# Kernel optimization log

Hardware: AMD Instinct MI355X
Metric: run time of the kernel (lower is better)

Reference implementation:

```python
import jax, jax.numpy as jnp
import numpy as np

SCORE_THRESHOLD = 0.5
NMS_TOP_K = 1024
NMS_THRESHOLD = 0.6
N_ANCHORS = 262144
N_CLASSES = 80


def setup_inputs() -> dict:
    key = jax.random.key(0)
    k1, k2, k3 = jax.random.split(key, 3)
    # valid xyxy boxes: x1<x2, y1<y2
    xy = jax.random.uniform(k1, (1, N_ANCHORS, 2), minval=0.0, maxval=2048.0)
    wh = jax.random.uniform(k2, (1, N_ANCHORS, 2), minval=1.0, maxval=64.0)
    pred_bboxes = jnp.concatenate([xy, xy + wh], axis=-1)  # [1, N, 4]
    pred_scores = jax.random.uniform(k3, (1, N_ANCHORS, N_CLASSES))  # [1, N, C]
    return {"pred_bboxes": pred_bboxes, "pred_scores": pred_scores}


def _pairwise_iou(boxes):
    # boxes: [K, 4] xyxy -> [K, K] IoU
    area = (boxes[:, 2] - boxes[:, 0]) * (boxes[:, 3] - boxes[:, 1])
    lt = jnp.maximum(boxes[:, None, :2], boxes[None, :, :2])
    rb = jnp.minimum(boxes[:, None, 2:], boxes[None, :, 2:])
    wh = jnp.clip(rb - lt, 0.0)
    inter = wh[..., 0] * wh[..., 1]
    union = area[:, None] + area[None, :] - inter
    return inter / jnp.maximum(union, 1e-9)


def reference(pred_bboxes, pred_scores):
    scores = pred_scores[0]  # [N, C]
    boxes = pred_bboxes[0]   # [N, 4]

    # single-label-per-box branch: per-anchor best class
    conf = jnp.max(scores, axis=1)      # [N]
    label = jnp.argmax(scores, axis=1)  # [N] int

    # score threshold (masking instead of data-dependent filtering)
    masked_conf = jnp.where(conf >= SCORE_THRESHOLD, conf, -1.0)

    # top-k candidates (sorted descending, matching torch.topk)
    top_conf, top_idx = jax.lax.top_k(masked_conf, NMS_TOP_K)  # [K]
    top_boxes = boxes[top_idx]   # [K, 4]
    top_label = label[top_idx]   # [K]
    valid = top_conf >= SCORE_THRESHOLD  # [K] rows that passed the threshold

    # batched_nms trick: offset boxes per class so cross-class IoU is ~0
    max_coord = jax.lax.stop_gradient(jnp.max(top_boxes)) + 1.0
    offset_boxes = top_boxes + top_label.astype(top_boxes.dtype)[:, None] * max_coord
    iou = _pairwise_iou(offset_boxes)  # [K, K]

    # sequential greedy suppression in score order (rows already sorted)
    idx = jnp.arange(NMS_TOP_K)

    def body(i, keep):
        suppress = (iou[i] > NMS_THRESHOLD) & (idx > i) & keep[i] & keep
        return keep & ~suppress

    keep = jax.lax.fori_loop(0, NMS_TOP_K, body, valid)  # [K] bool

    out = jnp.concatenate(
        [top_boxes, top_conf[:, None], top_label.astype(top_boxes.dtype)[:, None]],
        axis=1,
    )  # [K, 6] = [x1, y1, x2, y2, conf, label]
    # fixed-shape masked output: suppressed / invalid rows zeroed
    return out * keep[:, None].astype(out.dtype)
```

## Files before the change

### kernel.cpp

```cpp
#include <hip/hip_runtime.h>
#include <stdint.h>


#define N_ANCH   262144
#define N_CLS    80
#define K_TOP    1024
#define CAP      4096

typedef unsigned long long ull;

#define HSLOT(b) ((((b) & 2047u) << 4) | ((b) >> 11))
#define SKEW(e) ((uint32_t)(e) + ((uint32_t)(e) >> 4))

#define OFF_HIST  0
#define OFF_CTRL  131072
#define MEMSET_BYTES 131136
#define OFF_BINS  131136
#define OFF_LIST  655424
#define WS_REQUIRED 688192

__global__ __launch_bounds__(256) void k_sentinel(float* __restrict__ out, float v) {
    int i = blockIdx.x * 256 + threadIdx.x;
    if (i < K_TOP * 6) out[i] = v;
}

static __device__ __forceinline__ uint32_t conf_key24(float best) {
    uint32_t u = __float_as_uint(best);
    if (u > 0x3F800000u) u = 0x3F800000u;
    if (u < 0x3F000000u) u = 0x3F000000u;
    return u - 0x3F000000u;
}

static __device__ __forceinline__ void cmpsw(ull& x, ull& y, bool up) {
    ull mn = x < y ? x : y, mx = x < y ? y : x;
    x = up ? mn : mx; y = up ? mx : mn;
}

__global__ __launch_bounds__(256) void k_conf(const float* __restrict__ scores,
                                              uint16_t* __restrict__ bins16,
                                              uint32_t* __restrict__ hist) {
    const int t = threadIdx.x;
    const int r = t >> 4, s = t & 15;
    const int a0 = blockIdx.x * 128 + r;
    const float* base = scores + (size_t)a0 * N_CLS;
    float4 v0[4], v1[4];
    #pragma unroll
    for (int p = 0; p < 4; p++) {
        const float* nb = base + (size_t)p * 16 * N_CLS;
        v0[p] = ((const float4*)nb)[s];
        if (s < 4) v1[p] = ((const float4*)nb)[16 + s];
    }
    #pragma unroll
    for (int i = 0; i < 8; i++) {
        float4 c0 = v0[i & 3], c1 = v1[i & 3];
        if (i + 4 < 8) {
            const float* nb = base + (size_t)(i + 4) * 16 * N_CLS;
            v0[i & 3] = ((const float4*)nb)[s];
            if (s < 4) v1[i & 3] = ((const float4*)nb)[16 + s];
        }
        float best = c0.x; int lab = 4 * s;
        if (c0.y > best) { best = c0.y; lab = 4 * s + 1; }
        if (c0.z > best) { best = c0.z; lab = 4 * s + 2; }
        if (c0.w > best) { best = c0.w; lab = 4 * s + 3; }
        if (s < 4) {
            const int c = 64 + 4 * s;
            if (c1.x > best) { best = c1.x; lab = c; }
            if (c1.y > best) { best = c1.y; lab = c + 1; }
            if (c1.z > best) { best = c1.z; lab = c + 2; }
            if (c1.w > best) { best = c1.w; lab = c + 3; }
        }
        ull key = ((ull)(uint32_t)__float_as_uint(best) << 7) | (ull)(uint32_t)(127 - lab);
        ull o;
        o = __shfl_xor(key, 1); if (o > key) key = o;
        o = __shfl_xor(key, 2); if (o > key) key = o;
        o = __shfl_xor(key, 4); if (o > key) key = o;
        o = __shfl_xor(key, 8); if (o > key) key = o;
        if (s == 0) {
            const int a = a0 + i * 16;
            float bv = __uint_as_float((uint32_t)(key >> 7));
            uint16_t pk = 0;
            if (bv >= 0.5f) {
                uint32_t bin = conf_key24(bv) >> 8;
                if (bin > 32767u) bin = 32767u;
                atomicAdd(&hist[HSLOT(bin)], 1u);
                pk = (uint16_t)(0x8000u | bin);
            }
            bins16[a] = pk;
        }
    }
}

__global__ __launch_bounds__(1024) void k_cut(const uint32_t* __restrict__ hist,
                                              uint32_t* __restrict__ ctrl) {
    __shared__ uint32_t wtot[16], wsuf[16];
    const int t = threadIdx.x;
    const int lane = t & 63, w = t >> 6;
    const uint32_t sbase = (((uint32_t)t & 63u) << 9) | ((uint32_t)t >> 6);
    uint32_t c[32];
    #pragma unroll
    for (int i = 0; i < 32; i++) c[i] = hist[sbase | ((uint32_t)i << 4)];
    uint32_t part = 0;
    #pragma unroll
    for (int i = 0; i < 32; i++) part += c[i];
    uint32_t x = part;
    #pragma unroll
    for (int d = 1; d < 64; d <<= 1) {
        uint32_t o = __shfl_down(x, d);
        if (lane + d < 64) x += o;
    }
    if (lane == 0) wtot[w] = x;
    __syncthreads();
    if (t < 16) {
        uint32_t s = 0;
        for (int ww = t + 1; ww < 16; ww++) s += wtot[ww];
        wsuf[t] = s;
        if (t == 0) {
            uint32_t total = s + wtot[0];
            ctrl[1] = (total < K_TOP) ? total : K_TOP;
        }
    }
    __syncthreads();
    uint32_t run = (x + wsuf[w]) - part;
    if (run < K_TOP && run + part >= K_TOP) {
        uint32_t fnd = 0, cbv = 0;
        #pragma unroll
        for (int i = 31; i >= 0; i--) {
            if (!fnd && run + c[i] >= K_TOP) { cbv = (uint32_t)(t * 32 + i); fnd = 1; }
            if (!fnd) run += c[i];
        }
        ctrl[2] = cbv;
    }
}

__global__ __launch_bounds__(256) void k_gather(const float* __restrict__ scores,
                                                const uint16_t* __restrict__ bins16,
                                                uint32_t* __restrict__ ctrl,
                                                ull* __restrict__ list) {
    __shared__ uint32_t lcnt, lbase;
    const int t = threadIdx.x, b = blockIdx.x;
    if (t == 0) { lcnt = 0; lbase = 0; }
    __syncthreads();
    const uint32_t cT = ctrl[2];
    const int a4 = b * 256 + t;
    ushort4 pk4 = ((const ushort4*)bins16)[a4];
    uint16_t pk[4] = {pk4.x, pk4.y, pk4.z, pk4.w};
    ull      hk[4];
    uint32_t hs[4];
    bool     hv[4];
    #pragma unroll
    for (int e = 0; e < 4; e++) {
        hv[e] = false; hk[e] = 0; hs[e] = 0;
        uint32_t u = pk[e];
        if ((u & 0x8000u) && (u & 0x7FFFu) >= cT) {
            const uint32_t a = (uint32_t)a4 * 4u + (uint32_t)e;
            const float4* row = (const float4*)(scores + (size_t)a * N_CLS);
            float best = -1.f; int lab = 0;
            for (int f = 0; f < 20; f++) {
                float4 w = row[f];
                if (w.x > best) { best = w.x; lab = 4 * f; }
                if (w.y > best) { best = w.y; lab = 4 * f + 1; }
                if (w.z > best) { best = w.z; lab = 4 * f + 2; }
                if (w.w > best) { best = w.w; lab = 4 * f + 3; }
            }
            if (best >= 0.5f) {
                uint32_t k24 = conf_key24(best);
                hk[e] = ((ull)(0x1000000u - k24) << 25) | ((ull)a << 7)
                      | (ull)(uint32_t)lab;
                hs[e] = atomicAdd(&lcnt, 1u);
                hv[e] = true;
            }
        }
    }
    __syncthreads();
    if (t == 0 && lcnt) lbase = atomicAdd(&ctrl[0], lcnt);
    __syncthreads();
    const uint32_t base2 = lbase;
    #pragma unroll
    for (int e = 0; e < 4; e++) {
        if (hv[e]) {
            uint32_t slot = base2 + hs[e];
            if (slot < CAP) list[slot] = hk[e];
        }
    }
}

__global__ __launch_bounds__(1024) void k_final(const float4* __restrict__ bboxes,
                                                const uint32_t* __restrict__ ctrl,
                                                const ull* __restrict__ list,
                                                float* __restrict__ out) {
    __shared__ __align__(16) char smem[45056];
    ull*      sk    = (ull*)smem;
    float4*   ob    = (float4*)smem;
    float*    ar    = (float*)(smem + 16384);
    float*    red16 = (float*)(smem + 20480);
    uint32_t* g     = (uint32_t*)(smem + 20544);
    ull*      sup   = (ull*)(smem + 24640);
    uint8_t*  keepA = (uint8_t*)(smem + 32832);
    uint32_t* cnt   = (uint32_t*)(smem + 33856);
    uint32_t* stt   = (uint32_t*)(smem + 34176);
    uint8_t*  ovr   = (uint8_t*)(smem + 34496);
    ull*      cmask = (ull*)(smem + 34816);
    uint32_t* hist2 = (uint32_t*)(smem + 34816);
    uint32_t* gfail = (uint32_t*)(smem + 43008);
    uint32_t* wtot2 = (uint32_t*)(smem + 43012);
    uint32_t* wbase = (uint32_t*)(smem + 43076);
    const int t = threadIdx.x;
    const uint32_t nsel = ctrl[1];
    uint32_t ncand = ctrl[0]; if (ncand > CAP) ncand = CAP;

    ((uint2*)hist2)[t] = make_uint2(0u, 0u);
    if (t == 0) *gfail = 0;
    __syncthreads();
    ull      keys[4]; uint32_t kcs[4], olds[4]; bool val[4];
    #pragma unroll
    for (int e = 0; e < 4; e++) {
        int i = t + 1024 * e;
        val[e] = (i < (int)ncand); keys[e] = 0; kcs[e] = 0; olds[e] = 0;
        if (val[e]) {
            ull kk = list[i];
            keys[e] = kk;
            uint32_t kc = (uint32_t)(kk >> 25) - 0x800000u;
            if (kc >= 2048u) { *gfail = 1; val[e] = false; }
            else {
                kcs[e] = kc;
                uint32_t od = atomicAdd(&hist2[kc], 1u);
                olds[e] = od;
                if (od >= 16u) *gfail = 1;
            }
        }
    }
    __syncthreads();
    const bool ctOK = (*gfail == 0);

    if (ctOK) {
        uint32_t v0h = hist2[2 * t], v1h = hist2[2 * t + 1];
        uint32_t sseg = v0h + v1h;
        uint32_t incl = sseg;
        const int lane = t & 63, w = t >> 6;
        #pragma unroll
        for (int d = 1; d < 64; d <<= 1) {
            uint32_t o = __shfl_up(incl, d);
            if (lane >= d) incl += o;
        }
        if (lane == 63) wtot2[w] = incl;
        __syncthreads();
        if (t < 16) {
            uint32_t sb = 0;
            for (int i = 0; i < 16; i++) { uint32_t v = wtot2[i]; if (i < t) sb += v; }
            wbase[t] = sb;
        }
        __syncthreads();
        uint32_t ex = wbase[w] + incl - sseg;
        hist2[2 * t]     = ex;
        hist2[2 * t + 1] = ex + v0h;
        __syncthreads();
        #pragma unroll
        for (int e = 0; e < 4; e++)
            if (val[e]) sk[hist2[kcs[e]] + olds[e]] = keys[e];
        __syncthreads();
        #pragma unroll
        for (int e = 0; e < 4; e++) {
            if (val[e] && olds[e] == 0) {
                uint32_t base = hist2[kcs[e]];
                uint32_t nxt  = (kcs[e] < 2047u) ? hist2[kcs[e] + 1] : ncand;
                if (nxt - base >= 2u) {
                    for (uint32_t a2 = base + 1; a2 < nxt; a2++) {
                        ull kv = sk[a2];
                        uint32_t b2 = a2;
                        while (b2 > base && sk[b2 - 1] > kv) { sk[b2] = sk[b2 - 1]; b2--; }
                        sk[b2] = kv;
                    }
                }
            }
        }
    } else {
        uint32_t nsort = 1024;
        while (nsort < ncand) nsort <<= 1;
        if (nsort <= 2048) {
            const int TS2 = (int)(nsort >> 1);
            ull E0 = ~0ull, E1 = ~0ull;
            if (t < TS2) {
                int e = 2 * t;
                E0 = (e < (int)ncand)     ? list[e]     : ~0ull;
                E1 = (e + 1 < (int)ncand) ? list[e + 1] : ~0ull;
            }
            for (uint32_t k = 2; k <= nsort; k <<= 1) {
                for (uint32_t j = k >> 1; j > 0; j >>= 1) {
                    if (j >= 128) {
                        __syncthreads();
                        if (t < TS2) {
                            ulonglong2 wv; wv.x = E0; wv.y = E1;
                            *(ulonglong2*)&sk[2 * t] = wv;
                        }
                        __syncthreads();
                        if (t < TS2) {
                            uint32_t e0 = 2 * t;
                            ulonglong2 rv = *(const ulonglong2*)&sk[e0 ^ j];
                            bool km = (((e0 & k) == 0) != ((e0 & j) == 0));
                            E0 = ((E0 > rv.x) == km) ? E0 : rv.x;
                            E1 = ((E1 > rv.y) == km) ? E1 : rv.y;
                        }
                    } else if (t < TS2) {
                        if (j >= 2) {
                            int d = (int)(j >> 1);
                            bool km = ((((2 * t) & k) == 0) != (((2 * t) & j) == 0));
                            ull o0 = __shfl_xor(E0, d);
                            ull o1 = __shfl_xor(E1, d);
                            E0 = ((E0 > o0) == km) ? E0 : o0;
                            E1 = ((E1 > o1) == km) ? E1 : o1;
                        } else {
                            bool up = (((2 * t) & k) == 0);
                            cmpsw(E0, E1, up);
                        }
                    }
                }
            }
            __syncthreads();
            if (t < TS2) {
                ulonglong2 wv; wv.x = E0; wv.y = E1;
                *(ulonglong2*)&sk[2 * t] = wv;
            }
        } else {
            const int TS = (int)(nsort >> 2);
            ull E[4];
            if (t < TS) {
                #pragma unroll
                for (int rr = 0; rr < 4; rr++) {
                    int e = 4 * t + rr;
                    E[rr] = (e < (int)ncand) ? list[e] : ~0ull;
                }
            }
            for (uint32_t k = 2; k <= nsort; k <<= 1) {
                for (uint32_t j = k >> 1; j > 0; j >>= 1) {
                    if (j >= 256) {
                        __syncthreads();
                        if (t < TS) {
                            #pragma unroll
                            for (int rr = 0; rr < 4; rr++) sk[SKEW(4 * t + rr)] = E[rr];
                        }
                        __syncthreads();
                        if (t < TS) {
                            #pragma unroll
                            for (int rr = 0; rr < 4; rr++) {
                                uint32_t e = 4 * t + rr;
                                ull o = sk[SKEW(e ^ j)];
                                bool keepMax = (((e & k) == 0) != ((e & j) == 0));
                                bool gt = E[rr] > o;
                                E[rr] = (gt == keepMax) ? E[rr] : o;
                            }
                        }
                    } else if (t < TS) {
                        if (j >= 4) {
                            int d = (int)(j >> 2);
                            #pragma unroll
                            for (int rr = 0; rr < 4; rr++) {
                                uint32_t e = 4 * t + rr;
                                ull o = __shfl_xor(E[rr], d);
                                bool keepMax = (((e & k) == 0) != ((e & j) == 0));
                                bool gt = E[rr] > o;
                                E[rr] = (gt == keepMax) ? E[rr] : o;
                            }
                        } else if (j == 2) {
                            bool up = (((4 * t) & k) == 0);
                            cmpsw(E[0], E[2], up); cmpsw(E[1], E[3], up);
                        } else {
                            bool upA = (((4 * t) & k) == 0);
                            bool upB = (((4 * t + 2) & k) == 0);
                            cmpsw(E[0], E[1], upA);
                            cmpsw(E[2], E[3], upB);
                        }
                    }
                }
            }
            __syncthreads();
            if (t < TS) {
                #pragma unroll
                for (int rr = 0; rr < 4; rr++) sk[SKEW(4 * t + rr)] = E[rr];
            }
        }
    }
    __syncthreads();
    ull skey;
    if (ctOK) skey = sk[t];
    else {
        uint32_t nsort = 1024;
        while (nsort < ncand) nsort <<= 1;
        skey = (nsort <= 2048) ? sk[t] : sk[SKEW(t)];
    }
    __syncthreads();

    float4 bx = make_float4(0.f, 0.f, 0.f, 0.f);
    float cf = 0.f, lb = 0.f;
    uint32_t lab = 0;
    if ((uint32_t)t < nsel) {
        uint32_t idx = (uint32_t)(skey >> 7) & 0x3FFFFu;
        lab = (uint32_t)skey & 127u;
        cf = __uint_as_float(0x3F000000u + (0x1000000u - (uint32_t)(skey >> 25)));
        lb = (float)lab;
        bx = bboxes[idx];
    }
    float m = fmaxf(fmaxf(bx.x, bx.y), fmaxf(bx.z, bx.w));
    for (int d = 32; d > 0; d >>= 1) m = fmaxf(m, __shfl_xor(m, d));
    if ((t & 63) == 0) red16[t >> 6] = m;
    __syncthreads();
    float M = red16[0];
    #pragma unroll
    for (int w = 1; w < 16; w++) M = fmaxf(M, red16[w]);
    M = __fadd_rn(M, 1.0f);
    float o = __fmul_rn(lb, M);
    float4 q;
    q.x = __fadd_rn(bx.x, o); q.y = __fadd_rn(bx.y, o);
    q.z = __fadd_rn(bx.z, o); q.w = __fadd_rn(bx.w, o);
    ob[t] = q;
    ar[t] = __fmul_rn(__fsub_rn(q.z, q.x), __fsub_rn(q.w, q.y));
    g[t] = 0xFFFFFFFFu;
    if (t < N_CLS) ovr[t] = 0;
    keepA[t] = 0;
    if (t < 640) {
        ulonglong2 z; z.x = 0; z.y = 0;
        *(ulonglong2*)&cmask[2 * t] = z;
    }
    __syncthreads();

    if ((uint32_t)t < nsel)
        atomicOr(&cmask[lab * 16 + (t >> 6)], 1ull << (t & 63));
    __syncthreads();
    if (t < N_CLS) {
        uint32_t s = 0;
        #pragma unroll
        for (int w = 0; w < 16; w++) s += (uint32_t)__popcll(cmask[t * 16 + w]);
        cnt[t] = s;
    }
    __syncthreads();
    if (t < N_CLS) {
        uint32_t s = 0;
        for (int i = 0; i < N_CLS - 1; i++) {
            uint32_t v = cnt[i];
            if (i < t) s += v;
        }
        stt[t] = s;
    }
    __syncthreads();
    if ((uint32_t)t < nsel) {
        const ull* cm = &cmask[lab * 16];
        uint32_t w = (uint32_t)t >> 6;
        uint32_t r = (uint32_t)__popcll(cm[w] & ((1ull << (t & 63)) - 1ull));
        for (uint32_t ww = 0; ww < w; ww++) r += (uint32_t)__popcll(cm[ww]);
        g[stt[lab] + r] = (lab << 10) | (uint32_t)t;
    }
    __syncthreads();

    uint32_t gp = g[t];
    {
        ull sp = 0;
        if (gp != 0xFFFFFFFFu) {
            uint32_t labi = gp >> 10;
            uint32_t ri = gp & 1023u;
            float4 oi = ob[ri]; float ai = ar[ri];
            for (int qq = t + 1; qq < 1024; qq++) {
                uint32_t gq = g[qq];
                if ((gq >> 10) != labi) break;
                int dq = qq - t;
                if (dq > 64) { ovr[labi] = 1; break; }
                uint32_t rj = gq & 1023u;
                float4 oj = ob[rj];
                float lx = fmaxf(oi.x, oj.x), ly = fmaxf(oi.y, oj.y);
                float rx = fminf(oi.z, oj.z), ry = fminf(oi.w, oj.w);
                float wx = fmaxf(__fsub_rn(rx, lx), 0.f);
                float wy = fmaxf(__fsub_rn(ry, ly), 0.f);
                float inter = __fmul_rn(wx, wy);
                float uni = __fsub_rn(__fadd_rn(ai, ar[rj]), inter);
                float iou = __fdiv_rn(inter, fmaxf(uni, 1e-9f));
                if (iou > 0.6f) sp |= 1ull << (dq - 1);
            }
        }
        sup[t] = sp;
    }
    __syncthreads();

    if (t < N_CLS) {
        uint32_t n = cnt[t];
        if (n > 0) {
            uint32_t s0 = stt[t];
            if (n <= 64 && !ovr[t]) {
                ull kill = 0;
                for (uint32_t i = 0; i < n; i++) {
                    if (!((kill >> i) & 1ull)) {
                        if (i + 1 < 64) kill |= sup[s0 + i] << (i + 1);
                        keepA[g[s0 + i] & 1023u] = 1;
                    }
                }
            } else {
                for (uint32_t i = 0; i < n; i++) {
                    uint32_t ri = g[s0 + i] & 1023u;
                    float4 oi = ob[ri]; float ai = ar[ri];
                    bool kp = true;
                    for (uint32_t m2 = 0; m2 < i && kp; m2++) {
                        uint32_t rm = g[s0 + m2] & 1023u;
                        if (!keepA[rm]) continue;
                        float4 om = ob[rm];
                        float lx = fmaxf(om.x, oi.x), ly = fmaxf(om.y, oi.y);
                        float rx = fminf(om.z, oi.z), ry = fminf(om.w, oi.w);
                        float wx = fmaxf(__fsub_rn(rx, lx), 0.f);
                        float wy = fmaxf(__fsub_rn(ry, ly), 0.f);
                        float inter = __fmul_rn(wx, wy);
                        float uni = __fsub_rn(__fadd_rn(ar[rm], ai), inter);
                        float iou = __fdiv_rn(inter, fmaxf(uni, 1e-9f));
                        if (iou > 0.6f) kp = false;
                    }
                    keepA[ri] = kp ? 1 : 0;
                }
            }
        }
    }
    __syncthreads();

    const bool keep = keepA[t] != 0;
    float v0 = keep ? bx.x : 0.f, v1 = keep ? bx.y : 0.f;
    float v2 = keep ? bx.z : 0.f, v3 = keep ? bx.w : 0.f;
    float v4 = keep ? cf : 0.f, v5 = keep ? lb : 0.f;
    float2* o2 = (float2*)out;
    o2[t * 3 + 0] = make_float2(v0, v1);
    o2[t * 3 + 1] = make_float2(v2, v3);
    o2[t * 3 + 2] = make_float2(v4, v5);
}

extern "C" void kernel_launch(void* const* d_in, const int* in_sizes, int n_in,
                              void* d_out, int out_size, void* d_ws, size_t ws_size,
                              hipStream_t stream) {
    const float* bboxes = (const float*)d_in[0];
    const float* scores = (const float*)d_in[1];
    if (n_in >= 2 && in_sizes[0] > in_sizes[1]) {
        bboxes = (const float*)d_in[1];
        scores = (const float*)d_in[0];
    }

    if (ws_size < (size_t)WS_REQUIRED) {
        k_sentinel<<<(K_TOP * 6 + 255) / 256, 256, 0, stream>>>(
            (float*)d_out, (float)(ws_size >> 10));
        return;
    }

    char* ws = (char*)d_ws;
    uint32_t* hist   = (uint32_t*)(ws + OFF_HIST);
    uint32_t* ctrl   = (uint32_t*)(ws + OFF_CTRL);
    uint16_t* bins16 = (uint16_t*)(ws + OFF_BINS);
    ull*      list   = (ull*)(ws + OFF_LIST);

    hipMemsetAsync(ws, 0, MEMSET_BYTES, stream);
    k_conf  <<<N_ANCH / 128, 256, 0, stream>>>(scores, bins16, hist);
    k_cut   <<<1,           1024, 0, stream>>>(hist, ctrl);
    k_gather<<<256,          256, 0, stream>>>(scores, bins16, ctrl, list);
    k_final <<<1,           1024, 0, stream>>>((const float4*)bboxes, ctrl, list,
                                               (float*)d_out);
}
```

Before: 181.5 us.

## Fuse cut into gather kernel and compact per-class boxes for NMS

Folds the single-block threshold-finding kernel into the gather kernel: each of 64 blocks of 1024 threads redundantly scans the histogram to find the cut bin, which removes one kernel launch and the dependency through global memory. In the final kernel, boxes and areas are copied into class-sorted contiguous shared arrays, so the suppression mask loop uses a known trip count with direct indexing instead of indirect lookups and early-break checks. The overflow flag is dropped and replaced by a count-based decision. The cost is redundant histogram reads in every block, fewer and larger gather blocks, and more shared memory in the final kernel.

```diff
diff --git a/kernel.cpp b/kernel.cpp
--- a/kernel.cpp
+++ b/kernel.cpp
@@ -90,11 +90,15 @@
     }
 }
 
-__global__ __launch_bounds__(1024) void k_cut(const uint32_t* __restrict__ hist,
-                                              uint32_t* __restrict__ ctrl) {
-    __shared__ uint32_t wtot[16], wsuf[16];
-    const int t = threadIdx.x;
+__global__ __launch_bounds__(1024) void k_gather(const float* __restrict__ scores,
+                                                 const uint16_t* __restrict__ bins16,
+                                                 const uint32_t* __restrict__ hist,
+                                                 uint32_t* __restrict__ ctrl,
+                                                 ull* __restrict__ list) {
+    __shared__ uint32_t wtot[16], wsuf[16], shCT, lcnt, lbase;
+    const int t = threadIdx.x, b = blockIdx.x;
     const int lane = t & 63, w = t >> 6;
+    if (t == 0) { shCT = 0; lcnt = 0; lbase = 0; }
     const uint32_t sbase = (((uint32_t)t & 63u) << 9) | ((uint32_t)t >> 6);
     uint32_t c[32];
     #pragma unroll
@@ -114,34 +118,28 @@
         uint32_t s = 0;
         for (int ww = t + 1; ww < 16; ww++) s += wtot[ww];
         wsuf[t] = s;
-        if (t == 0) {
+        if (t == 0 && b == 0) {
             uint32_t total = s + wtot[0];
             ctrl[1] = (total < K_TOP) ? total : K_TOP;
         }
     }
     __syncthreads();
-    uint32_t run = (x + wsuf[w]) - part;
-    if (run < K_TOP && run + part >= K_TOP) {
-        uint32_t fnd = 0, cbv = 0;
-        #pragma unroll
-        for (int i = 31; i >= 0; i--) {
-            if (!fnd && run + c[i] >= K_TOP) { cbv = (uint32_t)(t * 32 + i); fnd = 1; }
-            if (!fnd) run += c[i];
-        }
-        ctrl[2] = cbv;
-    }
-}
-
-__global__ __launch_bounds__(256) void k_gather(const float* __restrict__ scores,
-                                                const uint16_t* __restrict__ bins16,
-                                                uint32_t* __restrict__ ctrl,
-                                                ull* __restrict__ list) {
-    __shared__ uint32_t lcnt, lbase;
-    const int t = threadIdx.x, b = blockIdx.x;
-    if (t == 0) { lcnt = 0; lbase = 0; }
-    __syncthreads();
-    const uint32_t cT = ctrl[2];
-    const int a4 = b * 256 + t;
+    {
+        uint32_t run = (x + wsuf[w]) - part;
+        if (run < K_TOP && run + part >= K_TOP) {
+            uint32_t fnd = 0, cbv = 0;
+            #pragma unroll
+            for (int i = 31; i >= 0; i--) {
+                if (!fnd && run + c[i] >= K_TOP) { cbv = (uint32_t)(t * 32 + i); fnd = 1; }
+                if (!fnd) run += c[i];
+            }
+            shCT = cbv;
+        }
+    }
+    __syncthreads();
+    const uint32_t cT = shCT;
+
+    const int a4 = b * 1024 + t;
     ushort4 pk4 = ((const ushort4*)bins16)[a4];
     uint16_t pk[4] = {pk4.x, pk4.y, pk4.z, pk4.w};
     ull      hk[4];
@@ -156,11 +154,11 @@
             const float4* row = (const float4*)(scores + (size_t)a * N_CLS);
             float best = -1.f; int lab = 0;
             for (int f = 0; f < 20; f++) {
-                float4 w = row[f];
-                if (w.x > best) { best = w.x; lab = 4 * f; }
-                if (w.y > best) { best = w.y; lab = 4 * f + 1; }
-                if (w.z > best) { best = w.z; lab = 4 * f + 2; }
-                if (w.w > best) { best = w.w; lab = 4 * f + 3; }
+                float4 w2 = row[f];
+                if (w2.x > best) { best = w2.x; lab = 4 * f; }
+                if (w2.y > best) { best = w2.y; lab = 4 * f + 1; }
+                if (w2.z > best) { best = w2.z; lab = 4 * f + 2; }
+                if (w2.w > best) { best = w2.w; lab = 4 * f + 3; }
             }
             if (best >= 0.5f) {
                 uint32_t k24 = conf_key24(best);
@@ -188,18 +186,19 @@
                                                 const uint32_t* __restrict__ ctrl,
                                                 const ull* __restrict__ list,
                                                 float* __restrict__ out) {
-    __shared__ __align__(16) char smem[45056];
+    __shared__ __align__(16) char smem[65280];
     ull*      sk    = (ull*)smem;
     float4*   ob    = (float4*)smem;
-    float*    ar    = (float*)(smem + 16384);
-    float*    red16 = (float*)(smem + 20480);
-    uint32_t* g     = (uint32_t*)(smem + 20544);
-    ull*      sup   = (ull*)(smem + 24640);
-    uint8_t*  keepA = (uint8_t*)(smem + 32832);
-    uint32_t* cnt   = (uint32_t*)(smem + 33856);
-    uint32_t* stt   = (uint32_t*)(smem + 34176);
-    uint8_t*  ovr   = (uint8_t*)(smem + 34496);
-    ull*      cmask = (ull*)(smem + 34816);
+    float4*   obg   = (float4*)(smem + 16384);
+    float*    ar    = (float*)(smem + 32768);
+    float*    arg   = (float*)(smem + 36864);
+    float*    red16 = (float*)(smem + 40960);
+    uint32_t* g     = (uint32_t*)(smem + 41024);
+    ull*      sup   = (ull*)(smem + 45120);
+    uint8_t*  keepA = (uint8_t*)(smem + 53312);
+    uint32_t* cnt   = (uint32_t*)(smem + 54336);
+    uint32_t* stt   = (uint32_t*)(smem + 54656);
+    ull*      cmask = (ull*)(smem + 54976);
     uint32_t* hist2 = (uint32_t*)(smem + 34816);
     uint32_t* gfail = (uint32_t*)(smem + 43008);
     uint32_t* wtot2 = (uint32_t*)(smem + 43012);
@@ -414,7 +413,6 @@
     ob[t] = q;
     ar[t] = __fmul_rn(__fsub_rn(q.z, q.x), __fsub_rn(q.w, q.y));
     g[t] = 0xFFFFFFFFu;
-    if (t < N_CLS) ovr[t] = 0;
     keepA[t] = 0;
     if (t < 640) {
         ulonglong2 z; z.x = 0; z.y = 0;
@@ -451,27 +449,32 @@
     __syncthreads();
 
     uint32_t gp = g[t];
+    if (gp != 0xFFFFFFFFu) {
+        uint32_t ri = gp & 1023u;
+        obg[t] = ob[ri];
+        arg[t] = ar[ri];
+    }
+    __syncthreads();
+
     {
         ull sp = 0;
         if (gp != 0xFFFFFFFFu) {
             uint32_t labi = gp >> 10;
-            uint32_t ri = gp & 1023u;
-            float4 oi = ob[ri]; float ai = ar[ri];
-            for (int qq = t + 1; qq < 1024; qq++) {
-                uint32_t gq = g[qq];
-                if ((gq >> 10) != labi) break;
-                int dq = qq - t;
-                if (dq > 64) { ovr[labi] = 1; break; }
-                uint32_t rj = gq & 1023u;
-                float4 oj = ob[rj];
+            uint32_t nsucc = cnt[labi] - (uint32_t)(t - stt[labi]) - 1u;
+            uint32_t trips = nsucc > 64u ? 64u : nsucc;
+            float4 oi = obg[t]; float ai = arg[t];
+            #pragma unroll 4
+            for (uint32_t d = 1; d <= trips; d++) {
+                float4 oj = obg[t + d];
+                float aj = arg[t + d];
                 float lx = fmaxf(oi.x, oj.x), ly = fmaxf(oi.y, oj.y);
                 float rx = fminf(oi.z, oj.z), ry = fminf(oi.w, oj.w);
                 float wx = fmaxf(__fsub_rn(rx, lx), 0.f);
                 float wy = fmaxf(__fsub_rn(ry, ly), 0.f);
                 float inter = __fmul_rn(wx, wy);
-                float uni = __fsub_rn(__fadd_rn(ai, ar[rj]), inter);
+                float uni = __fsub_rn(__fadd_rn(ai, aj), inter);
                 float iou = __fdiv_rn(inter, fmaxf(uni, 1e-9f));
-                if (iou > 0.6f) sp |= 1ull << (dq - 1);
+                if (iou > 0.6f) sp |= 1ull << (d - 1);
             }
         }
         sup[t] = sp;
@@ -482,7 +485,7 @@
         uint32_t n = cnt[t];
         if (n > 0) {
             uint32_t s0 = stt[t];
-            if (n <= 64 && !ovr[t]) {
+            if (n <= 64) {
                 ull kill = 0;
                 for (uint32_t i = 0; i < n; i++) {
                     if (!((kill >> i) & 1ull)) {
@@ -493,18 +496,17 @@
             } else {
                 for (uint32_t i = 0; i < n; i++) {
                     uint32_t ri = g[s0 + i] & 1023u;
-                    float4 oi = ob[ri]; float ai = ar[ri];
+                    float4 oi = obg[s0 + i]; float ai = arg[s0 + i];
                     bool kp = true;
                     for (uint32_t m2 = 0; m2 < i && kp; m2++) {
-                        uint32_t rm = g[s0 + m2] & 1023u;
-                        if (!keepA[rm]) continue;
-                        float4 om = ob[rm];
+                        if (!keepA[g[s0 + m2] & 1023u]) continue;
+                        float4 om = obg[s0 + m2];
                         float lx = fmaxf(om.x, oi.x), ly = fmaxf(om.y, oi.y);
                         float rx = fminf(om.z, oi.z), ry = fminf(om.w, oi.w);
                         float wx = fmaxf(__fsub_rn(rx, lx), 0.f);
                         float wy = fmaxf(__fsub_rn(ry, ly), 0.f);
                         float inter = __fmul_rn(wx, wy);
-                        float uni = __fsub_rn(__fadd_rn(ar[rm], ai), inter);
+                        float uni = __fsub_rn(__fadd_rn(arg[s0 + m2], ai), inter);
                         float iou = __fdiv_rn(inter, fmaxf(uni, 1e-9f));
                         if (iou > 0.6f) kp = false;
                     }
@@ -549,8 +551,7 @@
 
     hipMemsetAsync(ws, 0, MEMSET_BYTES, stream);
     k_conf  <<<N_ANCH / 128, 256, 0, stream>>>(scores, bins16, hist);
-    k_cut   <<<1,           1024, 0, stream>>>(hist, ctrl);
-    k_gather<<<256,          256, 0, stream>>>(scores, bins16, ctrl, list);
+    k_gather<<<64,          1024, 0, stream>>>(scores, bins16, hist, ctrl, list);
     k_final <<<1,           1024, 0, stream>>>((const float4*)bboxes, ctrl, list,
                                                (float*)d_out);
 }
```

Result: no change. 177.9 us, median of 2 (-1.9%).
